# Optimization experiments

Measured on AMD Instinct MI355X. Metric: run time of the kernel, lower is better.

Reference implementation:

```python
import jax, jax.numpy as jnp
import numpy as np
from jax import lax

B, T, N = 32, 48, 360   # batch, time steps, ROIs
H = 100                 # LSTM hidden (self.L)
D = 64                  # attention hidden (self.D)
K = 1                   # attention heads (self.K)
NUM_CLASS = 2


def setup_inputs() -> dict:
    key = jax.random.key(0)
    ks = jax.random.split(key, 14)
    s = 0.02
    return {
        "x": jax.random.normal(ks[0], (B, T, N, N), dtype=jnp.float32),
        # GCN: Linear(ROInum, 1) applied to (x @ I)
        "w_gcn": jax.random.normal(ks[1], (N,), dtype=jnp.float32) * s,
        "b_gcn": jnp.zeros((), dtype=jnp.float32),
        # LSTM (pytorch layout: [4H, in] with gate order i,f,g,o)
        "W_ih": jax.random.normal(ks[2], (4 * H, N), dtype=jnp.float32) * s,
        "W_hh": jax.random.normal(ks[3], (4 * H, H), dtype=jnp.float32) * s,
        "b_ih": jnp.zeros((4 * H,), dtype=jnp.float32),
        "b_hh": jnp.zeros((4 * H,), dtype=jnp.float32),
        # attention MLP: Linear(L,D) -> tanh -> Linear(D,K)
        "wa1": jax.random.normal(ks[4], (D, H), dtype=jnp.float32) * s,
        "ba1": jnp.zeros((D,), dtype=jnp.float32),
        "wa2": jax.random.normal(ks[5], (K, D), dtype=jnp.float32) * s,
        "ba2": jnp.zeros((K,), dtype=jnp.float32),
        # classifier: Linear(L*K, num_class) -> softmax (dropout inactive at eval)
        "wc": jax.random.normal(ks[6], (NUM_CLASS, H * K), dtype=jnp.float32) * s,
        "bc": jnp.zeros((NUM_CLASS,), dtype=jnp.float32),
    }


def _lstm(seq, W_ih, W_HH, b):
    # seq: [B, T, N] -> hidden states [B, T, H]
    def step(carry, xt):
        h, c = carry
        gates = xt @ W_ih.T + h @ W_HH.T + b  # [B, 4H]
        i, f, g, o = jnp.split(gates, 4, axis=-1)
        i, f, o = jax.nn.sigmoid(i), jax.nn.sigmoid(f), jax.nn.sigmoid(o)
        c = f * c + i * jnp.tanh(g)
        h = o * jnp.tanh(c)
        return (h, c), h

    h0 = jnp.zeros((seq.shape[0], H), seq.dtype)
    c0 = jnp.zeros((seq.shape[0], H), seq.dtype)
    _, hs = lax.scan(step, (h0, c0), jnp.swapaxes(seq, 0, 1))
    return jnp.swapaxes(hs, 0, 1)


def reference(x, w_gcn, b_gcn, W_ih, W_hh, b_ih, b_hh, wa1, ba1, wa2, ba2, wc, bc):
    # GCN per (sample, timestep): h = relu(Linear(x @ I)) == relu(x @ w + b)
    # batched over B and T in one einsum (eliminates the python loops).
    gout = jax.nn.relu(jnp.einsum("btnm,m->btn", x, w_gcn) + b_gcn)  # [B,T,N]

    out = _lstm(gout, W_ih, W_hh, b_ih + b_hh)  # [B,T,H]

    # MIL attention: A = Linear(tanh(Linear(out)))
    A = jnp.tanh(jnp.einsum("bth,dh->btd", out, wa1) + ba1)
    A = jnp.einsum("btd,kd->btk", A, wa2) + ba2          # [B,T,K]
    A = jnp.swapaxes(A, 2, 1)                             # [B,K,T]
    Att = A
    A = jax.nn.softmax(A, axis=2)
    M = jnp.einsum("bkt,bth->bkh", A, out).reshape(x.shape[0], H * K)

    Y_prob = jax.nn.softmax(M @ wc.T + bc, axis=1)  # dropout is identity at eval
    return (Y_prob, Att)
```

## Files before the change

kernel.cpp:

```cpp
#include <hip/hip_runtime.h>
#include <math.h>

#define BB 32
#define TT 48
#define NN 360
#define HH 100
#define DD 64
#define NC 2
#define G4 (4*HH)

__device__ __forceinline__ float sigmoid_fast(float x) {
    return 1.f / (1.f + __expf(-x));
}
__device__ __forceinline__ float tanh_fast(float x) {
    float ax = fabsf(x);
    float e = __expf(-2.f * ax);
    float t = (1.f - e) / (1.f + e);
    return copysignf(t, x);
}
__device__ __forceinline__ float dot4(float4 a, float4 b) {
    return a.x*b.x + a.y*b.y + a.z*b.z + a.w*b.w;
}
__device__ __forceinline__ float bcast_lane(float v, int l) {
    return __int_as_float(__builtin_amdgcn_readlane(__float_as_int(v), l));
}

__global__ __launch_bounds__(256) void gcn_kernel(const float* __restrict__ x,
                                                  const float* __restrict__ w,
                                                  const float* __restrict__ bptr,
                                                  float* __restrict__ gout, int nquads) {
    __shared__ __align__(16) float4 w4[90];
    int tid = threadIdx.x;
    if (tid < 90) w4[tid] = ((const float4*)w)[tid];
    __syncthreads();
    float b = bptr[0];
    int lane = tid & 63;
    int wv = tid >> 6;
    int stride = 4 * gridDim.x;
    for (int q = blockIdx.x * 4 + wv; q < nquads; q += stride) {
        int row0 = 4 * q;
        const float4* x0 = (const float4*)(x + (size_t)(row0 + 0) * NN);
        const float4* x1 = (const float4*)(x + (size_t)(row0 + 1) * NN);
        const float4* x2 = (const float4*)(x + (size_t)(row0 + 2) * NN);
        const float4* x3 = (const float4*)(x + (size_t)(row0 + 3) * NN);
        float4 a0 = x0[lane];
        float4 a1 = x1[lane];
        float4 a2 = x2[lane];
        float4 a3 = x3[lane];
        float4 wa = w4[lane];
        float p0 = dot4(a0, wa);
        float p1 = dot4(a1, wa);
        float p2 = dot4(a2, wa);
        float p3 = dot4(a3, wa);
        if (lane < 26) {
            float4 b0 = x0[lane + 64];
            float4 b1 = x1[lane + 64];
            float4 b2 = x2[lane + 64];
            float4 b3 = x3[lane + 64];
            float4 wb = w4[lane + 64];
            p0 += dot4(b0, wb);
            p1 += dot4(b1, wb);
            p2 += dot4(b2, wb);
            p3 += dot4(b3, wb);
        }
        #pragma unroll
        for (int off = 32; off; off >>= 1) {
            p0 += __shfl_down(p0, off, 64);
            p1 += __shfl_down(p1, off, 64);
            p2 += __shfl_down(p2, off, 64);
            p3 += __shfl_down(p3, off, 64);
        }
        if (lane == 0) {
            float4 r;
            r.x = fmaxf(p0 + b, 0.f);
            r.y = fmaxf(p1 + b, 0.f);
            r.z = fmaxf(p2 + b, 0.f);
            r.w = fmaxf(p3 + b, 0.f);
            ((float4*)gout)[q] = r;
        }
    }
}

__global__ void transpose_wih(const float* __restrict__ Wih, float* __restrict__ Wt) {
    int idx = blockIdx.x * blockDim.x + threadIdx.x;
    if (idx < NN * G4) {
        int n = idx / G4, j = idx % G4;
        Wt[idx] = Wih[j * NN + n];
    }
}

#define BT2 4
__global__ __launch_bounds__(512) void xproj_kernel(const float* __restrict__ gout,
                                                    const float* __restrict__ Wt,
                                                    const float* __restrict__ b_ih,
                                                    const float* __restrict__ b_hh,
                                                    float* __restrict__ xproj) {
    __shared__ __align__(16) float gt[BT2 * NN];
    int bt0 = blockIdx.x * BT2;
    int tid = threadIdx.x;
    for (int i = tid; i < BT2 * NN; i += 512) gt[i] = gout[bt0 * NN + i];
    __syncthreads();
    if (tid < G4) {
        float a0 = 0.f, a1 = 0.f, a2 = 0.f, a3 = 0.f;
        for (int n = 0; n < NN; n += 8) {
            float w0 = Wt[(n+0)*G4 + tid];
            float w1 = Wt[(n+1)*G4 + tid];
            float w2 = Wt[(n+2)*G4 + tid];
            float w3 = Wt[(n+3)*G4 + tid];
            float w4_ = Wt[(n+4)*G4 + tid];
            float w5 = Wt[(n+5)*G4 + tid];
            float w6 = Wt[(n+6)*G4 + tid];
            float w7 = Wt[(n+7)*G4 + tid];
            #pragma unroll
            for (int i = 0; i < 1; i++) {}
            float4 g0a = *(const float4*)&gt[0*NN + n];
            float4 g0b = *(const float4*)&gt[0*NN + n + 4];
            float4 g1a = *(const float4*)&gt[1*NN + n];
            float4 g1b = *(const float4*)&gt[1*NN + n + 4];
            float4 g2a = *(const float4*)&gt[2*NN + n];
            float4 g2b = *(const float4*)&gt[2*NN + n + 4];
            float4 g3a = *(const float4*)&gt[3*NN + n];
            float4 g3b = *(const float4*)&gt[3*NN + n + 4];
            a0 += g0a.x*w0 + g0a.y*w1 + g0a.z*w2 + g0a.w*w3
                + g0b.x*w4_ + g0b.y*w5 + g0b.z*w6 + g0b.w*w7;
            a1 += g1a.x*w0 + g1a.y*w1 + g1a.z*w2 + g1a.w*w3
                + g1b.x*w4_ + g1b.y*w5 + g1b.z*w6 + g1b.w*w7;
            a2 += g2a.x*w0 + g2a.y*w1 + g2a.z*w2 + g2a.w*w3
                + g2b.x*w4_ + g2b.y*w5 + g2b.z*w6 + g2b.w*w7;
            a3 += g3a.x*w0 + g3a.y*w1 + g3a.z*w2 + g3a.w*w3
                + g3b.x*w4_ + g3b.y*w5 + g3b.z*w6 + g3b.w*w7;
        }
        float bias = b_ih[tid] + b_hh[tid];
        xproj[(size_t)(bt0 + 0) * G4 + tid] = a0 + bias;
        xproj[(size_t)(bt0 + 1) * G4 + tid] = a1 + bias;
        xproj[(size_t)(bt0 + 2) * G4 + tid] = a2 + bias;
        xproj[(size_t)(bt0 + 3) * G4 + tid] = a3 + bias;
    }
}

__global__ __launch_bounds__(448) void lstm_attn_kernel(const float* __restrict__ xproj,
                                                        const float* __restrict__ Whh,
                                                        const float* __restrict__ wa1,
                                                        const float* __restrict__ ba1,
                                                        const float* __restrict__ wa2,
                                                        const float* __restrict__ ba2,
                                                        const float* __restrict__ wc,
                                                        const float* __restrict__ bc,
                                                        float* __restrict__ out) {
    __shared__ __align__(16) float ho[TT * HH];
    __shared__ __align__(16) float h_lds[128];
    __shared__ float gates[G4];
    __shared__ float sc[TT];
    __shared__ float p[TT];
    __shared__ float M[HH];
    int b = blockIdx.x;
    int tid = threadIdx.x;
    int lane = tid & 63;
    float wr[HH];
    if (tid < G4) {
        #pragma unroll
        for (int k = 0; k < HH; k++) wr[k] = Whh[tid * HH + k];
    }
    float c = 0.f;
    if (tid < 128) h_lds[tid] = 0.f;
    float xp = (tid < G4) ? xproj[(size_t)(b * TT) * G4 + tid] : 0.f;
    __syncthreads();
    for (int t = 0; t < TT; t++) {
        float xp_next = (tid < G4 && t + 1 < TT)
                      ? xproj[(size_t)(b * TT + t + 1) * G4 + tid] : 0.f;
        float ha = h_lds[lane];
        float hb = h_lds[64 + lane];
        if (tid < G4) {
            float s0 = 0.f, s1 = 0.f, s2 = 0.f, s3 = 0.f;
            #pragma unroll
            for (int k = 0; k < 64; k += 4) {
                s0 += bcast_lane(ha, k+0) * wr[k+0];
                s1 += bcast_lane(ha, k+1) * wr[k+1];
                s2 += bcast_lane(ha, k+2) * wr[k+2];
                s3 += bcast_lane(ha, k+3) * wr[k+3];
            }
            #pragma unroll
            for (int k = 64; k < 100; k += 4) {
                s0 += bcast_lane(hb, k-64) * wr[k+0];
                s1 += bcast_lane(hb, k-63) * wr[k+1];
                s2 += bcast_lane(hb, k-62) * wr[k+2];
                s3 += bcast_lane(hb, k-61) * wr[k+3];
            }
            gates[tid] = xp + (s0 + s1) + (s2 + s3);
        }
        __syncthreads();
        if (tid < HH) {
            float ig = sigmoid_fast(gates[tid]);
            float fg = sigmoid_fast(gates[tid + HH]);
            float gg = tanh_fast(gates[tid + 2*HH]);
            float og = sigmoid_fast(gates[tid + 3*HH]);
            c = fg * c + ig * gg;
            float hh = og * tanh_fast(c);
            h_lds[tid] = hh;
            ho[t * HH + tid] = hh;
        }
        xp = xp_next;
        __syncthreads();
    }
    int wave = tid >> 6;
    for (int t = wave; t < TT; t += 7) {
        float a = 0.f;
        if (lane < DD) {
            float s = ba1[lane];
            #pragma unroll
            for (int h2 = 0; h2 < HH; h2 += 4) {
                float4 h4v = *(const float4*)&ho[t*HH + h2];
                s += wa1[lane*HH + h2+0]*h4v.x + wa1[lane*HH + h2+1]*h4v.y
                   + wa1[lane*HH + h2+2]*h4v.z + wa1[lane*HH + h2+3]*h4v.w;
            }
            a = tanh_fast(s) * wa2[lane];
        }
        #pragma unroll
        for (int off = 32; off; off >>= 1) a += __shfl_down(a, off, 64);
        if (lane == 0) sc[t] = a + ba2[0];
    }
    __syncthreads();
    if (tid < 64) {
        float v = (lane < TT) ? sc[lane] : -1e30f;
        if (lane < TT) out[BB*NC + b*TT + lane] = v;
        float m = v;
        #pragma unroll
        for (int off = 32; off; off >>= 1) m = fmaxf(m, __shfl_xor(m, off, 64));
        float e = (lane < TT) ? __expf(v - m) : 0.f;
        float s = e;
        #pragma unroll
        for (int off = 32; off; off >>= 1) s += __shfl_xor(s, off, 64);
        if (lane < TT) p[lane] = e / s;
    }
    __syncthreads();
    if (tid < HH) {
        float m = 0.f;
        #pragma unroll
        for (int t = 0; t < TT; t++) m += p[t] * ho[t*HH + tid];
        M[tid] = m;
    }
    __syncthreads();
    if (tid == 0) {
        float l0 = bc[0], l1 = bc[1];
        for (int h2 = 0; h2 < HH; h2++) { l0 += M[h2]*wc[h2]; l1 += M[h2]*wc[HH + h2]; }
        float mx = fmaxf(l0, l1);
        float e0 = __expf(l0 - mx), e1 = __expf(l1 - mx);
        float s = e0 + e1;
        out[b*NC + 0] = e0 / s;
        out[b*NC + 1] = e1 / s;
    }
}

extern "C" void kernel_launch(void* const* d_in, const int* in_sizes, int n_in,
                              void* d_out, int out_size, void* d_ws, size_t ws_size,
                              hipStream_t stream) {
    const float* x     = (const float*)d_in[0];
    const float* w_gcn = (const float*)d_in[1];
    const float* b_gcn = (const float*)d_in[2];
    const float* W_ih  = (const float*)d_in[3];
    const float* W_hh  = (const float*)d_in[4];
    const float* b_ih  = (const float*)d_in[5];
    const float* b_hh  = (const float*)d_in[6];
    const float* wa1   = (const float*)d_in[7];
    const float* ba1   = (const float*)d_in[8];
    const float* wa2   = (const float*)d_in[9];
    const float* ba2   = (const float*)d_in[10];
    const float* wc    = (const float*)d_in[11];
    const float* bc    = (const float*)d_in[12];
    float* out = (float*)d_out;
    float* ws  = (float*)d_ws;

    float* gout  = ws;
    float* Wt    = gout + 552960;
    float* xproj = Wt + 144000;

    int nquads = BB * TT * NN / 4;
    transpose_wih<<<(NN*G4 + 255)/256, 256, 0, stream>>>(W_ih, Wt);
    gcn_kernel<<<2048, 256, 0, stream>>>(x, w_gcn, b_gcn, gout, nquads);
    xproj_kernel<<<(BB*TT)/BT2, 512, 0, stream>>>(gout, Wt, b_ih, b_hh, xproj);
    lstm_attn_kernel<<<BB, 448, 0, stream>>>(xproj, W_hh, wa1, ba1, wa2, ba2, wc, bc, out);
}
```

Baseline: 238.4 us.

## Fuse weight transpose, GCN and input projection into one kernel with grid barrier

```diff
diff --git a/kernel.cpp b/kernel.cpp
--- a/kernel.cpp
+++ b/kernel.cpp
@@ -7,7 +7,9 @@
 #define HH 100
 #define DD 64
 #define NC 2
-#define G4 (4*HH)
+#define G4 400
+#define GRID_A 2048
+#define XPROJ_BLOCKS 384
 
 __device__ __forceinline__ float sigmoid_fast(float x) {
     return 1.f / (1.f + __expf(-x));
@@ -25,116 +27,122 @@
     return __int_as_float(__builtin_amdgcn_readlane(__float_as_int(v), l));
 }
 
-__global__ __launch_bounds__(256) void gcn_kernel(const float* __restrict__ x,
-                                                  const float* __restrict__ w,
-                                                  const float* __restrict__ bptr,
-                                                  float* __restrict__ gout, int nquads) {
+__global__ __launch_bounds__(256, 4) void fusedA_kernel(const float* __restrict__ x,
+                                                        const float* __restrict__ w_gcn,
+                                                        const float* __restrict__ bptr,
+                                                        const float* __restrict__ W_ih,
+                                                        const float* __restrict__ b_ih,
+                                                        const float* __restrict__ b_hh,
+                                                        float* __restrict__ gout,
+                                                        float* __restrict__ Wt2,
+                                                        float* __restrict__ xproj,
+                                                        unsigned* __restrict__ bar) {
     __shared__ __align__(16) float4 w4[90];
     int tid = threadIdx.x;
-    if (tid < 90) w4[tid] = ((const float4*)w)[tid];
-    __syncthreads();
-    float b = bptr[0];
-    int lane = tid & 63;
-    int wv = tid >> 6;
-    int stride = 4 * gridDim.x;
-    for (int q = blockIdx.x * 4 + wv; q < nquads; q += stride) {
-        int row0 = 4 * q;
-        const float4* x0 = (const float4*)(x + (size_t)(row0 + 0) * NN);
-        const float4* x1 = (const float4*)(x + (size_t)(row0 + 1) * NN);
-        const float4* x2 = (const float4*)(x + (size_t)(row0 + 2) * NN);
-        const float4* x3 = (const float4*)(x + (size_t)(row0 + 3) * NN);
-        float4 a0 = x0[lane];
-        float4 a1 = x1[lane];
-        float4 a2 = x2[lane];
-        float4 a3 = x3[lane];
-        float4 wa = w4[lane];
-        float p0 = dot4(a0, wa);
-        float p1 = dot4(a1, wa);
-        float p2 = dot4(a2, wa);
-        float p3 = dot4(a3, wa);
-        if (lane < 26) {
-            float4 b0 = x0[lane + 64];
-            float4 b1 = x1[lane + 64];
-            float4 b2 = x2[lane + 64];
-            float4 b3 = x3[lane + 64];
-            float4 wb = w4[lane + 64];
-            p0 += dot4(b0, wb);
-            p1 += dot4(b1, wb);
-            p2 += dot4(b2, wb);
-            p3 += dot4(b3, wb);
-        }
-        #pragma unroll
-        for (int off = 32; off; off >>= 1) {
-            p0 += __shfl_down(p0, off, 64);
-            p1 += __shfl_down(p1, off, 64);
-            p2 += __shfl_down(p2, off, 64);
-            p3 += __shfl_down(p3, off, 64);
-        }
-        if (lane == 0) {
-            float4 r;
-            r.x = fmaxf(p0 + b, 0.f);
-            r.y = fmaxf(p1 + b, 0.f);
-            r.z = fmaxf(p2 + b, 0.f);
-            r.w = fmaxf(p3 + b, 0.f);
-            ((float4*)gout)[q] = r;
-        }
-    }
-}
-
-__global__ void transpose_wih(const float* __restrict__ Wih, float* __restrict__ Wt) {
-    int idx = blockIdx.x * blockDim.x + threadIdx.x;
-    if (idx < NN * G4) {
-        int n = idx / G4, j = idx % G4;
-        Wt[idx] = Wih[j * NN + n];
-    }
-}
-
-#define BT2 4
-__global__ __launch_bounds__(512) void xproj_kernel(const float* __restrict__ gout,
-                                                    const float* __restrict__ Wt,
-                                                    const float* __restrict__ b_ih,
-                                                    const float* __restrict__ b_hh,
-                                                    float* __restrict__ xproj) {
-    __shared__ __align__(16) float gt[BT2 * NN];
-    int bt0 = blockIdx.x * BT2;
-    int tid = threadIdx.x;
-    for (int i = tid; i < BT2 * NN; i += 512) gt[i] = gout[bt0 * NN + i];
-    __syncthreads();
-    if (tid < G4) {
-        float a0 = 0.f, a1 = 0.f, a2 = 0.f, a3 = 0.f;
-        for (int n = 0; n < NN; n += 8) {
-            float w0 = Wt[(n+0)*G4 + tid];
-            float w1 = Wt[(n+1)*G4 + tid];
-            float w2 = Wt[(n+2)*G4 + tid];
-            float w3 = Wt[(n+3)*G4 + tid];
-            float w4_ = Wt[(n+4)*G4 + tid];
-            float w5 = Wt[(n+5)*G4 + tid];
-            float w6 = Wt[(n+6)*G4 + tid];
-            float w7 = Wt[(n+7)*G4 + tid];
-            #pragma unroll
-            for (int i = 0; i < 1; i++) {}
-            float4 g0a = *(const float4*)&gt[0*NN + n];
-            float4 g0b = *(const float4*)&gt[0*NN + n + 4];
-            float4 g1a = *(const float4*)&gt[1*NN + n];
-            float4 g1b = *(const float4*)&gt[1*NN + n + 4];
-            float4 g2a = *(const float4*)&gt[2*NN + n];
-            float4 g2b = *(const float4*)&gt[2*NN + n + 4];
-            float4 g3a = *(const float4*)&gt[3*NN + n];
-            float4 g3b = *(const float4*)&gt[3*NN + n + 4];
-            a0 += g0a.x*w0 + g0a.y*w1 + g0a.z*w2 + g0a.w*w3
-                + g0b.x*w4_ + g0b.y*w5 + g0b.z*w6 + g0b.w*w7;
-            a1 += g1a.x*w0 + g1a.y*w1 + g1a.z*w2 + g1a.w*w3
-                + g1b.x*w4_ + g1b.y*w5 + g1b.z*w6 + g1b.w*w7;
-            a2 += g2a.x*w0 + g2a.y*w1 + g2a.z*w2 + g2a.w*w3
-                + g2b.x*w4_ + g2b.y*w5 + g2b.z*w6 + g2b.w*w7;
-            a3 += g3a.x*w0 + g3a.y*w1 + g3a.z*w2 + g3a.w*w3
-                + g3b.x*w4_ + g3b.y*w5 + g3b.z*w6 + g3b.w*w7;
-        }
-        float bias = b_ih[tid] + b_hh[tid];
-        xproj[(size_t)(bt0 + 0) * G4 + tid] = a0 + bias;
-        xproj[(size_t)(bt0 + 1) * G4 + tid] = a1 + bias;
-        xproj[(size_t)(bt0 + 2) * G4 + tid] = a2 + bias;
-        xproj[(size_t)(bt0 + 3) * G4 + tid] = a3 + bias;
+    {
+        int idx = blockIdx.x * 256 + tid;
+        if (idx < NN * G4) {
+            int j = idx / NN, n = idx % NN;
+            Wt2[n * G4 + 2 * (j % 200) + (j / 200)] = W_ih[idx];
+        }
+    }
+    if (tid < 90) w4[tid] = ((const float4*)w_gcn)[tid];
+    __syncthreads();
+    {
+        float b = bptr[0];
+        int lane = tid & 63;
+        int wv = tid >> 6;
+        const int nquads = BB * TT * NN / 4;
+        const int stride = 4 * GRID_A;
+        for (int q = blockIdx.x * 4 + wv; q < nquads; q += stride) {
+            int row0 = 4 * q;
+            const float4* x0 = (const float4*)(x + (size_t)(row0 + 0) * NN);
+            const float4* x1 = (const float4*)(x + (size_t)(row0 + 1) * NN);
+            const float4* x2 = (const float4*)(x + (size_t)(row0 + 2) * NN);
+            const float4* x3 = (const float4*)(x + (size_t)(row0 + 3) * NN);
+            float4 a0 = x0[lane];
+            float4 a1 = x1[lane];
+            float4 a2 = x2[lane];
+            float4 a3 = x3[lane];
+            float4 wa = w4[lane];
+            float p0 = dot4(a0, wa);
+            float p1 = dot4(a1, wa);
+            float p2 = dot4(a2, wa);
+            float p3 = dot4(a3, wa);
+            if (lane < 26) {
+                float4 b0 = x0[lane + 64];
+                float4 b1 = x1[lane + 64];
+                float4 b2 = x2[lane + 64];
+                float4 b3 = x3[lane + 64];
+                float4 wb = w4[lane + 64];
+                p0 += dot4(b0, wb);
+                p1 += dot4(b1, wb);
+                p2 += dot4(b2, wb);
+                p3 += dot4(b3, wb);
+            }
+            #pragma unroll
+            for (int off = 32; off; off >>= 1) {
+                p0 += __shfl_down(p0, off, 64);
+                p1 += __shfl_down(p1, off, 64);
+                p2 += __shfl_down(p2, off, 64);
+                p3 += __shfl_down(p3, off, 64);
+            }
+            if (lane == 0) {
+                float4 r;
+                r.x = fmaxf(p0 + b, 0.f);
+                r.y = fmaxf(p1 + b, 0.f);
+                r.z = fmaxf(p2 + b, 0.f);
+                r.w = fmaxf(p3 + b, 0.f);
+                ((float4*)gout)[q] = r;
+            }
+        }
+    }
+    __syncthreads();
+    __threadfence();
+    if (tid == 0) atomicAdd(bar, 1u);
+    if (blockIdx.x >= XPROJ_BLOCKS) return;
+    if (tid == 0) {
+        while (atomicAdd(bar, 0u) < (unsigned)GRID_A) __builtin_amdgcn_s_sleep(8);
+    }
+    __syncthreads();
+    __threadfence();
+    if (tid < 200) {
+        int r0 = blockIdx.x * 4;
+        float acc00 = 0.f, acc01 = 0.f, acc10 = 0.f, acc11 = 0.f;
+        float acc20 = 0.f, acc21 = 0.f, acc30 = 0.f, acc31 = 0.f;
+        const float* g0p = gout + (size_t)(r0 + 0) * NN;
+        const float* g1p = gout + (size_t)(r0 + 1) * NN;
+        const float* g2p = gout + (size_t)(r0 + 2) * NN;
+        const float* g3p = gout + (size_t)(r0 + 3) * NN;
+        const float* wp = Wt2 + 2 * tid;
+        for (int n = 0; n < NN; n += 4) {
+            float4 g0 = *(const float4*)(g0p + n);
+            float4 g1 = *(const float4*)(g1p + n);
+            float4 g2 = *(const float4*)(g2p + n);
+            float4 g3 = *(const float4*)(g3p + n);
+            float2 wA = *(const float2*)(wp + (n + 0) * G4);
+            float2 wB = *(const float2*)(wp + (n + 1) * G4);
+            float2 wC = *(const float2*)(wp + (n + 2) * G4);
+            float2 wD = *(const float2*)(wp + (n + 3) * G4);
+            acc00 += g0.x*wA.x + g0.y*wB.x + g0.z*wC.x + g0.w*wD.x;
+            acc01 += g0.x*wA.y + g0.y*wB.y + g0.z*wC.y + g0.w*wD.y;
+            acc10 += g1.x*wA.x + g1.y*wB.x + g1.z*wC.x + g1.w*wD.x;
+            acc11 += g1.x*wA.y + g1.y*wB.y + g1.z*wC.y + g1.w*wD.y;
+            acc20 += g2.x*wA.x + g2.y*wB.x + g2.z*wC.x + g2.w*wD.x;
+            acc21 += g2.x*wA.y + g2.y*wB.y + g2.z*wC.y + g2.w*wD.y;
+            acc30 += g3.x*wA.x + g3.y*wB.x + g3.z*wC.x + g3.w*wD.x;
+            acc31 += g3.x*wA.y + g3.y*wB.y + g3.z*wC.y + g3.w*wD.y;
+        }
+        float bias0 = b_ih[tid] + b_hh[tid];
+        float bias1 = b_ih[tid + 200] + b_hh[tid + 200];
+        xproj[(size_t)(r0 + 0) * G4 + tid]       = acc00 + bias0;
+        xproj[(size_t)(r0 + 0) * G4 + tid + 200] = acc01 + bias1;
+        xproj[(size_t)(r0 + 1) * G4 + tid]       = acc10 + bias0;
+        xproj[(size_t)(r0 + 1) * G4 + tid + 200] = acc11 + bias1;
+        xproj[(size_t)(r0 + 2) * G4 + tid]       = acc20 + bias0;
+        xproj[(size_t)(r0 + 2) * G4 + tid + 200] = acc21 + bias1;
+        xproj[(size_t)(r0 + 3) * G4 + tid]       = acc30 + bias0;
+        xproj[(size_t)(r0 + 3) * G4 + tid + 200] = acc31 + bias1;
     }
 }
 
@@ -271,12 +279,12 @@
     float* ws  = (float*)d_ws;
 
     float* gout  = ws;
-    float* Wt    = gout + 552960;
-    float* xproj = Wt + 144000;
-
-    int nquads = BB * TT * NN / 4;
-    transpose_wih<<<(NN*G4 + 255)/256, 256, 0, stream>>>(W_ih, Wt);
-    gcn_kernel<<<2048, 256, 0, stream>>>(x, w_gcn, b_gcn, gout, nquads);
-    xproj_kernel<<<(BB*TT)/BT2, 512, 0, stream>>>(gout, Wt, b_ih, b_hh, xproj);
+    float* Wt2   = gout + 552960;
+    float* xproj = Wt2 + 144000;
+    unsigned* bar = (unsigned*)((char*)d_ws + (8u << 20));
+
+    hipMemsetAsync(bar, 0, 64, stream);
+    fusedA_kernel<<<GRID_A, 256, 0, stream>>>(x, w_gcn, b_gcn, W_ih, b_ih, b_hh,
+                                              gout, Wt2, xproj, bar);
     lstm_attn_kernel<<<BB, 448, 0, stream>>>(xproj, W_hh, wa1, ba1, wa2, ba2, wc, bc, out);
 }
```

After: 734.5 us. +208.1%, slower.
